# Kernel optimization log

Hardware: AMD Instinct MI355X
Metric: run time of the kernel (lower is better)

## Reference

```python
import jax, jax.numpy as jnp
import numpy as np

B, S, D, H = 2, 2048, 1024, 16
HD = D // H           # 64
AD = D // 8           # adapter dim 128


def setup_inputs() -> dict:
    key = jax.random.key(0)
    ks = jax.random.split(key, 16)
    s = 1.0 / np.sqrt(D)
    sa = 1.0 / np.sqrt(AD)
    return {
        "q": jax.random.normal(ks[0], (B, S, D), jnp.float32),
        "k": jax.random.normal(ks[1], (B, S, D), jnp.float32),
        "v": jax.random.normal(ks[2], (B, S, D), jnp.float32),
        "Wq": jax.random.normal(ks[3], (D, D), jnp.float32) * s,
        "bq": jnp.zeros((D,), jnp.float32),
        "Wk": jax.random.normal(ks[4], (D, D), jnp.float32) * s,
        "bk": jnp.zeros((D,), jnp.float32),
        "Wv": jax.random.normal(ks[5], (D, D), jnp.float32) * s,
        "bv": jnp.zeros((D,), jnp.float32),
        "Wo": jax.random.normal(ks[6], (D, D), jnp.float32) * s,
        "bo": jnp.zeros((D,), jnp.float32),
        "Wad": jax.random.normal(ks[7], (AD, D), jnp.float32) * s,
        "bad": jnp.zeros((AD,), jnp.float32),
        "Wau": jax.random.normal(ks[8], (D, AD), jnp.float32) * sa,
        "bau": jnp.zeros((D,), jnp.float32),
    }


def reference(q, k, v, Wq, bq, Wk, bk, Wv, bv, Wo, bo, Wad, bad, Wau, bau):
    # Linear projections (torch Linear: x @ W.T + b), split into heads
    def proj(x, W, b):
        y = jnp.einsum('bsd,ed->bse', x, W) + b
        return y.reshape(B, -1, H, HD).transpose(0, 2, 1, 3)  # [B,H,S,HD]

    qh, kh, vh = proj(q, Wq, bq), proj(k, Wk, bk), proj(v, Wv, bv)
    scores = jnp.einsum('bhqd,bhkd->bhqk', qh, kh) / np.sqrt(HD)  # [B,H,S,S]
    attn = jax.nn.softmax(scores, axis=-1)
    ctx = jnp.einsum('bhqk,bhkd->bhqd', attn, vh)
    ctx = ctx.transpose(0, 2, 1, 3).reshape(B, -1, D)  # [B,S,D]
    out = jnp.einsum('bsd,ed->bse', ctx, Wo) + bo
    # adapter: down -> GELU (exact erf) -> up, fused with residual
    a = jnp.einsum('bsd,ad->bsa', out, Wad) + bad
    a = jax.nn.gelu(a, approximate=False)
    a = jnp.einsum('bsa,da->bsd', a, Wau) + bau
    return out + a
```

## Files before the change

kernel.cpp:

```cpp
#include <hip/hip_runtime.h>
#include <hip/hip_bf16.h>
#include <math.h>

typedef __attribute__((ext_vector_type(8))) short short8;
typedef __attribute__((ext_vector_type(4))) float f32x4;

#define MFMA16(a,b,c) __builtin_amdgcn_mfma_f32_16x16x32_bf16((a),(b),(c),0,0,0)

__device__ __forceinline__ unsigned short f2bf(float f){
    union { __hip_bfloat16 b; unsigned short u; } cv;
    cv.b = __float2bfloat16(f);
    return cv.u;
}
__device__ __forceinline__ unsigned pk_bf16(float a, float b){
    unsigned r;
    asm("v_cvt_pk_bf16_f32 %0, %1, %2" : "=v"(r) : "v"(a), "v"(b));
    return r;
}
__device__ __forceinline__ float ex2(float x){
    return __builtin_amdgcn_exp2f(x);
}

#define GLD_LDS16(g, s) \
    __builtin_amdgcn_global_load_lds((const __attribute__((address_space(1))) void*)(g), \
                                     (__attribute__((address_space(3))) void*)(s), 16, 0, 0)

#define QSCALE 0.18033688011112042f
#define DEFER_THR 11.0f

struct CvtJobs {
    const float* src[6];
    unsigned short* dst[6];
    float scale[6];
    int n[6];
};

__global__ __launch_bounds__(256)
void convert_kernel(CvtJobs j, long long total4) {
    long long i4 = (long long)blockIdx.x * blockDim.x + threadIdx.x;
    if (i4 >= total4) return;
    long long rem = i4 * 4;
    int job = 0;
    while (job < 6 && rem >= j.n[job]) { rem -= j.n[job]; ++job; }
    if (job >= 6) return;
    const float sc = j.scale[job];
    const float4 v = *(const float4*)(j.src[job] + rem);
    ushort4 o;
    o.x = f2bf(v.x * sc); o.y = f2bf(v.y * sc);
    o.z = f2bf(v.z * sc); o.w = f2bf(v.w * sc);
    *(ushort4*)(j.dst[job] + rem) = o;
}

struct QKVArgs {
    const float* A[3];
    const unsigned short* W[3];
    const float* bias[3];
    float bscale[3];
    unsigned short* out[3];
};

__global__ __launch_bounds__(256)
void gemm_qkv(QKVArgs ar, int M, int N, int K)
{
    __shared__ float          Asf[2][128 * 32];
    __shared__ unsigned short Bs[2][128 * 32];

    const int z = blockIdx.z;
    const float* A = ar.A[z];
    const unsigned short* W = ar.W[z];
    const int tid = threadIdx.x;
    const int w = tid >> 6, l = tid & 63;
    const int lr = l & 15, lg = l >> 4;
    const int wr = w >> 1, wc = w & 1;
    const int m0 = blockIdx.x * 128, n0 = blockIdx.y * 128;
    const int ru = lg ^ ((lr >> 1) & 3);

    auto STAGE = [&](int bf, int k0) {
        #pragma unroll
        for (int c = 0; c < 4; ++c) {
            const int cid = c * 256 + tid;
            const int row = cid >> 3, u = cid & 7;
            const int su = u ^ (row & 7);
            GLD_LDS16((const char*)A + ((size_t)(m0 + row) * K + k0) * 4 + su * 16,
                      (char*)&Asf[bf][0] + (c * 256 + w * 64) * 16);
        }
        #pragma unroll
        for (int c = 0; c < 2; ++c) {
            const int cid = c * 256 + tid;
            const int row = cid >> 2, u = cid & 3;
            const int su = u ^ ((row >> 1) & 3);
            GLD_LDS16((const char*)W + ((size_t)(n0 + row) * K + k0) * 2 + su * 16,
                      (char*)&Bs[bf][0] + (c * 256 + w * 64) * 16);
        }
    };

    f32x4 acc[4][4] = {};
    STAGE(0, 0);
    __syncthreads();
    int cur = 0;

    for (int k0 = 0; k0 < K; k0 += 32) {
        if (k0 + 32 < K) STAGE(cur ^ 1, k0 + 32);

        short8 af[4], bfr[4];
        #pragma unroll
        for (int i = 0; i < 4; ++i) {
            const int row = wr * 64 + i * 16 + lr;
            const char* rb = (const char*)&Asf[cur][0] + row * 128;
            const float4 f0 = *(const float4*)(rb + (((lg * 2 + 0) ^ (row & 7)) * 16));
            const float4 f1 = *(const float4*)(rb + (((lg * 2 + 1) ^ (row & 7)) * 16));
            union { unsigned u[4]; short8 s; } cv;
            cv.u[0] = pk_bf16(f0.x, f0.y);
            cv.u[1] = pk_bf16(f0.z, f0.w);
            cv.u[2] = pk_bf16(f1.x, f1.y);
            cv.u[3] = pk_bf16(f1.z, f1.w);
            af[i] = cv.s;
        }
        #pragma unroll
        for (int jj = 0; jj < 4; ++jj)
            bfr[jj] = *(const short8*)((const char*)&Bs[cur][0] + (wc * 64 + jj * 16 + lr) * 64 + ru * 16);
        #pragma unroll
        for (int i = 0; i < 4; ++i)
            #pragma unroll
            for (int jj = 0; jj < 4; ++jj)
                acc[i][jj] = MFMA16(af[i], bfr[jj], acc[i][jj]);

        __syncthreads();
        cur ^= 1;
    }

    const float* bias = ar.bias[z];
    const float bsc = ar.bscale[z];
    unsigned short* out = ar.out[z];
    #pragma unroll
    for (int i = 0; i < 4; ++i)
        #pragma unroll
        for (int jj = 0; jj < 4; ++jj)
            #pragma unroll
            for (int r = 0; r < 4; ++r) {
                const int row = m0 + wr * 64 + i * 16 + lg * 4 + r;
                const int col = n0 + wc * 64 + jj * 16 + lr;
                const float c = acc[i][jj][r] + bias[col] * bsc;
                const int b = row >> 11, s = row & 2047, h = col >> 6, hd = col & 63;
                if (z < 2)
                    out[((((size_t)(b * 16 + h)) * 2048 + s) << 6) + hd] = f2bf(c);
                else
                    out[((((size_t)(b * 16 + h)) * 64 + hd) << 11) + s] = f2bf(c);
            }
}

template<int MODE>
__global__ __launch_bounds__(256)
void gemm_bf16(const unsigned short* __restrict__ A,
               const unsigned short* __restrict__ Wt,
               const float* __restrict__ bias,
               void* __restrict__ out0,
               void* __restrict__ out1,
               int M, int N, int K)
{
    __shared__ unsigned short As[2][128 * 32];
    __shared__ unsigned short Bs[2][128 * 32];

    const int tid = threadIdx.x;
    const int w = tid >> 6, l = tid & 63;
    const int lr = l & 15, lg = l >> 4;
    const int wr = w >> 1, wc = w & 1;
    const int m0 = blockIdx.x * 128, n0 = blockIdx.y * 128;
    const int ru = lg ^ ((lr >> 1) & 3);

    auto STAGE = [&](int bf, int k0) {
        #pragma unroll
        for (int c = 0; c < 2; ++c) {
            const int cid = c * 256 + tid;
            const int row = cid >> 2, u = cid & 3;
            const int su = u ^ ((row >> 1) & 3);
            GLD_LDS16((const char*)A  + ((size_t)(m0 + row) * K + k0) * 2 + su * 16,
                      (char*)&As[bf][0] + (c * 256 + w * 64) * 16);
            GLD_LDS16((const char*)Wt + ((size_t)(n0 + row) * K + k0) * 2 + su * 16,
                      (char*)&Bs[bf][0] + (c * 256 + w * 64) * 16);
        }
    };

    f32x4 acc[4][4] = {};
    STAGE(0, 0);
    __syncthreads();
    int cur = 0;

    for (int k0 = 0; k0 < K; k0 += 32) {
        if (k0 + 32 < K) STAGE(cur ^ 1, k0 + 32);

        short8 af[4], bfr[4];
        #pragma unroll
        for (int i = 0; i < 4; ++i)
            af[i] = *(const short8*)((const char*)&As[cur][0] + (wr * 64 + i * 16 + lr) * 64 + ru * 16);
        #pragma unroll
        for (int jj = 0; jj < 4; ++jj)
            bfr[jj] = *(const short8*)((const char*)&Bs[cur][0] + (wc * 64 + jj * 16 + lr) * 64 + ru * 16);
        #pragma unroll
        for (int i = 0; i < 4; ++i)
            #pragma unroll
            for (int jj = 0; jj < 4; ++jj)
                acc[i][jj] = MFMA16(af[i], bfr[jj], acc[i][jj]);

        __syncthreads();
        cur ^= 1;
    }

    #pragma unroll
    for (int i = 0; i < 4; ++i)
        #pragma unroll
        for (int jj = 0; jj < 4; ++jj)
            #pragma unroll
            for (int r = 0; r < 4; ++r) {
                const int row = m0 + wr * 64 + i * 16 + lg * 4 + r;
                const int col = n0 + wc * 64 + jj * 16 + lr;
                const float c = acc[i][jj][r] + bias[col];
                if (MODE == 2) {
                    ((float*)out0)[(size_t)row * N + col] = c;
                    ((unsigned short*)out1)[(size_t)row * N + col] = f2bf(c);
                } else {
                    ((float*)out0)[(size_t)row * N + col] =
                        c + ((const float*)out1)[(size_t)row * N + col];
                }
            }
}

__global__ __launch_bounds__(256)
void gemm64_gelu(const unsigned short* __restrict__ A,
                 const unsigned short* __restrict__ Wt,
                 const float* __restrict__ bias,
                 unsigned short* __restrict__ out,
                 int M, int N, int K)
{
    __shared__ unsigned short As[2][64 * 32];
    __shared__ unsigned short Bs[2][64 * 32];

    const int tid = threadIdx.x;
    const int w = tid >> 6, l = tid & 63;
    const int lr = l & 15, lg = l >> 4;
    const int wr = w >> 1, wc = w & 1;
    const int m0 = blockIdx.x * 64, n0 = blockIdx.y * 64;

    auto STAGE = [&](int bf, int k0) {
        const int row = tid >> 2, ch = tid & 3;
        GLD_LDS16(A  + (size_t)(m0 + row) * K + k0 + ch * 8, &As[bf][0] + (w * 64) * 8);
        GLD_LDS16(Wt + (size_t)(n0 + row) * K + k0 + ch * 8, &Bs[bf][0] + (w * 64) * 8);
    };

    f32x4 acc[2][2] = {};
    STAGE(0, 0);
    __syncthreads();
    int cur = 0;

    for (int k0 = 0; k0 < K; k0 += 32) {
        if (k0 + 32 < K) STAGE(cur ^ 1, k0 + 32);

        short8 af[2], bfr[2];
        #pragma unroll
        for (int i = 0; i < 2; ++i)
            af[i] = *(const short8*)(&As[cur][0] + ((wr * 32 + i * 16 + lr) * 32 + lg * 8));
        #pragma unroll
        for (int jj = 0; jj < 2; ++jj)
            bfr[jj] = *(const short8*)(&Bs[cur][0] + ((wc * 32 + jj * 16 + lr) * 32 + lg * 8));
        #pragma unroll
        for (int i = 0; i < 2; ++i)
            #pragma unroll
            for (int jj = 0; jj < 2; ++jj)
                acc[i][jj] = MFMA16(af[i], bfr[jj], acc[i][jj]);

        __syncthreads();
        cur ^= 1;
    }

    #pragma unroll
    for (int i = 0; i < 2; ++i)
        #pragma unroll
        for (int jj = 0; jj < 2; ++jj)
            #pragma unroll
            for (int r = 0; r < 4; ++r) {
                const int row = m0 + wr * 32 + i * 16 + lg * 4 + r;
                const int col = n0 + wc * 32 + jj * 16 + lr;
                const float c = acc[i][jj][r] + bias[col];
                const float g = 0.5f * c * (1.0f + erff(c * 0.70710678118654752f));
                out[(size_t)row * N + col] = f2bf(g);
            }
}

__global__ __launch_bounds__(512)
void attn_mfma(const unsigned short* __restrict__ Qh,
               const unsigned short* __restrict__ Kh,
               const unsigned short* __restrict__ Vt,
               unsigned short* __restrict__ ctx)
{
    __shared__ unsigned short Ks[2][64 * 64];
    __shared__ unsigned short Vs[2][64 * 64];
    __shared__ unsigned short Ps[8][16 * 64];

    const int tid = threadIdx.x;
    const int w = tid >> 6, l = tid & 63;
    const int lr = l & 15, lg = l >> 4;

    const int p = blockIdx.x + blockIdx.y * 16;
    const int id = (p & 7) * 64 + (p >> 3);
    const int q0 = (id & 15) << 7;
    const int bh = id >> 4;

    const unsigned short* Qb = Qh + (size_t)bh * 131072;
    const char* Kb = (const char*)(Kh + (size_t)bh * 131072);
    const char* Vb = (const char*)(Vt + (size_t)bh * 131072);

    short8 qf[2];
    #pragma unroll
    for (int c = 0; c < 2; ++c)
        qf[c] = *(const short8*)(Qb + (size_t)(q0 + w * 16 + lr) * 64 + c * 32 + lg * 8);

    float mrow = -1e30f;
    float lrow = 0.f;
    f32x4 accO[4] = {};

    auto STAGE = [&](int bf, int kt) {
        const int row = tid >> 3, u = tid & 7;
        const int su = u ^ (row & 7);
        GLD_LDS16(Kb + (size_t)(kt + row) * 128 + su * 16,
                  (char*)&Ks[bf][0] + (w * 64) * 16);
        GLD_LDS16(Vb + (size_t)row * 4096 + (size_t)kt * 2 + su * 16,
                  (char*)&Vs[bf][0] + (w * 64) * 16);
    };

    STAGE(0, 0);
    __syncthreads();

    int cur = 0;
    for (int t = 0; t < 32; ++t) {
        if (t < 31) STAGE(cur ^ 1, (t + 1) * 64);

        const char* Kbuf = (const char*)&Ks[cur][0];
        const char* Vbuf = (const char*)&Vs[cur][0];

        f32x4 sf[4] = {};
        __builtin_amdgcn_s_setprio(1);
        #pragma unroll
        for (int n = 0; n < 4; ++n) {
            const int krow = n * 16 + lr;
            const short8 kf0 = *(const short8*)(Kbuf + krow * 128 + ((0 * 4 + lg) ^ (lr & 7)) * 16);
            const short8 kf1 = *(const short8*)(Kbuf + krow * 128 + ((1 * 4 + lg) ^ (lr & 7)) * 16);
            sf[n] = MFMA16(kf0, qf[0], sf[n]);
            sf[n] = MFMA16(kf1, qf[1], sf[n]);
        }
        __builtin_amdgcn_s_setprio(0);

        short8 vf[4][2];
        #pragma unroll
        for (int n = 0; n < 4; ++n) {
            const int drow = n * 16 + lr;
            vf[n][0] = *(const short8*)(Vbuf + drow * 128 + ((0 * 4 + lg) ^ (lr & 7)) * 16);
            vf[n][1] = *(const short8*)(Vbuf + drow * 128 + ((1 * 4 + lg) ^ (lr & 7)) * 16);
        }

        float a = fmaxf(fmaxf(fmaxf(sf[0][0], sf[0][1]), fmaxf(sf[0][2], sf[0][3])),
                        fmaxf(fmaxf(sf[1][0], sf[1][1]), fmaxf(sf[1][2], sf[1][3])));
        float b2 = fmaxf(fmaxf(fmaxf(sf[2][0], sf[2][1]), fmaxf(sf[2][2], sf[2][3])),
                         fmaxf(fmaxf(sf[3][0], sf[3][1]), fmaxf(sf[3][2], sf[3][3])));
        float r2 = fmaxf(a, b2);
        r2 = fmaxf(r2, __shfl_xor(r2, 16));
        r2 = fmaxf(r2, __shfl_xor(r2, 32));
        const bool need = (r2 > mrow + DEFER_THR);
        if (__any(need)) {
            const float mnew = fmaxf(mrow, r2);
            const float rsc = ex2(mrow - mnew);
            lrow *= rsc;
            mrow = mnew;
            #pragma unroll
            for (int r = 0; r < 4; ++r) {
                const float rr = __shfl(rsc, (l & 48) | (lg * 4 + r));
                #pragma unroll
                for (int n = 0; n < 4; ++n) accO[n][r] *= rr;
            }
        }
        {
            const float m = mrow;
            float ls = lrow;
            char* pbase = (char*)&Ps[w][0] + lr * 128;
            #pragma unroll
            for (int n = 0; n < 4; ++n) {
                const float p0 = ex2(sf[n][0] - m);
                const float p1 = ex2(sf[n][1] - m);
                const float p2 = ex2(sf[n][2] - m);
                const float p3 = ex2(sf[n][3] - m);
                ls += (p0 + p1) + (p2 + p3);
                uint2 pk;
                pk.x = pk_bf16(p0, p1);
                pk.y = pk_bf16(p2, p3);
                *(uint2*)(pbase + (((n * 2 + (lg >> 1)) ^ (lr & 7)) * 16) + (lg & 1) * 8) = pk;
            }
            lrow = ls;
        }

        asm volatile("" ::: "memory");

        short8 pf[2];
        {
            const char* pb = (const char*)&Ps[w][0] + lr * 128;
            #pragma unroll
            for (int c = 0; c < 2; ++c) {
                union { uint2 q2[2]; short8 s8; } cvt;
                const char* base = pb + (((c * 4 + lg) ^ (lr & 7)) * 16);
                cvt.q2[0] = *(const uint2*)(base);
                cvt.q2[1] = *(const uint2*)(base + 8);
                pf[c] = cvt.s8;
            }
        }

        __builtin_amdgcn_s_setprio(1);
        #pragma unroll
        for (int n = 0; n < 4; ++n) {
            accO[n] = MFMA16(pf[0], vf[n][0], accO[n]);
            accO[n] = MFMA16(pf[1], vf[n][1], accO[n]);
        }
        __builtin_amdgcn_s_setprio(0);

        __syncthreads();
        cur ^= 1;
    }

    const int b = bh >> 4, h = bh & 15;
    {
        float ls = lrow;
        ls += __shfl_xor(ls, 16);
        ls += __shfl_xor(ls, 32);
        const float inv = 1.0f / ls;
        #pragma unroll
        for (int r = 0; r < 4; ++r) {
            const float vr = __shfl(inv, (l & 48) | (lg * 4 + r));
            const int srow = q0 + w * 16 + lg * 4 + r;
            const size_t base = ((size_t)b * 2048 + srow) * 1024 + h * 64;
            #pragma unroll
            for (int n = 0; n < 4; ++n)
                ctx[base + n * 16 + lr] = f2bf(accO[n][r] * vr);
        }
    }
}

extern "C" void kernel_launch(void* const* d_in, const int* in_sizes, int n_in,
                              void* d_out, int out_size, void* d_ws, size_t ws_size,
                              hipStream_t stream) {
    const float* q   = (const float*)d_in[0];
    const float* k   = (const float*)d_in[1];
    const float* v   = (const float*)d_in[2];
    const float* Wq  = (const float*)d_in[3];
    const float* bq  = (const float*)d_in[4];
    const float* Wk  = (const float*)d_in[5];
    const float* bk  = (const float*)d_in[6];
    const float* Wv  = (const float*)d_in[7];
    const float* bv  = (const float*)d_in[8];
    const float* Wo  = (const float*)d_in[9];
    const float* bo  = (const float*)d_in[10];
    const float* Wad = (const float*)d_in[11];
    const float* bad = (const float*)d_in[12];
    const float* Wau = (const float*)d_in[13];
    const float* bau = (const float*)d_in[14];

    const int M = 4096, D = 1024, AD = 128;
    const size_t SZ = (size_t)M * D;

    char* p = (char*)d_ws;
    size_t off = 0;
    auto alloc = [&](size_t bytes) { void* r = p + off; off = (off + bytes + 255) & ~(size_t)255; return r; };
    unsigned short* Wqb  = (unsigned short*)alloc((size_t)D * D * 2);
    unsigned short* Wkb  = (unsigned short*)alloc((size_t)D * D * 2);
    unsigned short* Wvb  = (unsigned short*)alloc((size_t)D * D * 2);
    unsigned short* Wob  = (unsigned short*)alloc((size_t)D * D * 2);
    unsigned short* Wadb = (unsigned short*)alloc((size_t)AD * D * 2);
    unsigned short* Waub = (unsigned short*)alloc((size_t)D * AD * 2);
    unsigned short* Qh   = (unsigned short*)alloc(SZ * 2);
    unsigned short* Kh   = (unsigned short*)alloc(SZ * 2);
    unsigned short* Vt   = (unsigned short*)alloc(SZ * 2);
    unsigned short* ctx  = (unsigned short*)alloc(SZ * 2);
    float*          outp = (float*)alloc(SZ * 4);
    unsigned short* outb = (unsigned short*)alloc(SZ * 2);
    unsigned short* a1   = (unsigned short*)alloc((size_t)M * AD * 2);

    CvtJobs j;
    j.src[0] = Wq;  j.dst[0] = Wqb;  j.n[0] = D * D;   j.scale[0] = QSCALE;
    j.src[1] = Wk;  j.dst[1] = Wkb;  j.n[1] = D * D;   j.scale[1] = 1.f;
    j.src[2] = Wv;  j.dst[2] = Wvb;  j.n[2] = D * D;   j.scale[2] = 1.f;
    j.src[3] = Wo;  j.dst[3] = Wob;  j.n[3] = D * D;   j.scale[3] = 1.f;
    j.src[4] = Wad; j.dst[4] = Wadb; j.n[4] = AD * D;  j.scale[4] = 1.f;
    j.src[5] = Wau; j.dst[5] = Waub; j.n[5] = D * AD;  j.scale[5] = 1.f;
    long long total = 4LL * D * D + 2LL * AD * D;
    long long total4 = total / 4;
    convert_kernel<<<dim3((unsigned)((total4 + 255) / 256)), dim3(256), 0, stream>>>(j, total4);

    const dim3 blk(256);

    QKVArgs qa;
    qa.A[0] = q;   qa.A[1] = k;   qa.A[2] = v;
    qa.W[0] = Wqb; qa.W[1] = Wkb; qa.W[2] = Wvb;
    qa.bias[0] = bq; qa.bias[1] = bk; qa.bias[2] = bv;
    qa.bscale[0] = QSCALE; qa.bscale[1] = 1.f; qa.bscale[2] = 1.f;
    qa.out[0] = Qh; qa.out[1] = Kh; qa.out[2] = Vt;
    gemm_qkv<<<dim3(M / 128, D / 128, 3), blk, 0, stream>>>(qa, M, D, D);

    attn_mfma<<<dim3(16, 32), dim3(512), 0, stream>>>(Qh, Kh, Vt, ctx);

    gemm_bf16<2><<<dim3(M / 128, D / 128), blk, 0, stream>>>(ctx, Wob, bo, outp, outb, M, D, D);
    gemm64_gelu<<<dim3(M / 64, AD / 64), blk, 0, stream>>>(outb, Wadb, bad, a1, M, AD, D);
    gemm_bf16<4><<<dim3(M / 128, D / 128), blk, 0, stream>>>(a1, Waub, bau, d_out, outp, M, D, AD);
}
```

Before: 153.4 us.

## Load QKV GEMM operands directly from global memory, dropping LDS staging

```diff
diff --git a/kernel.cpp b/kernel.cpp
--- a/kernel.cpp
+++ b/kernel.cpp
@@ -62,9 +62,6 @@
 __global__ __launch_bounds__(256)
 void gemm_qkv(QKVArgs ar, int M, int N, int K)
 {
-    __shared__ float          Asf[2][128 * 32];
-    __shared__ unsigned short Bs[2][128 * 32];
-
     const int z = blockIdx.z;
     const float* A = ar.A[z];
     const unsigned short* W = ar.W[z];
@@ -73,42 +70,24 @@
     const int lr = l & 15, lg = l >> 4;
     const int wr = w >> 1, wc = w & 1;
     const int m0 = blockIdx.x * 128, n0 = blockIdx.y * 128;
-    const int ru = lg ^ ((lr >> 1) & 3);
-
-    auto STAGE = [&](int bf, int k0) {
-        #pragma unroll
-        for (int c = 0; c < 4; ++c) {
-            const int cid = c * 256 + tid;
-            const int row = cid >> 3, u = cid & 7;
-            const int su = u ^ (row & 7);
-            GLD_LDS16((const char*)A + ((size_t)(m0 + row) * K + k0) * 4 + su * 16,
-                      (char*)&Asf[bf][0] + (c * 256 + w * 64) * 16);
-        }
-        #pragma unroll
-        for (int c = 0; c < 2; ++c) {
-            const int cid = c * 256 + tid;
-            const int row = cid >> 2, u = cid & 3;
-            const int su = u ^ ((row >> 1) & 3);
-            GLD_LDS16((const char*)W + ((size_t)(n0 + row) * K + k0) * 2 + su * 16,
-                      (char*)&Bs[bf][0] + (c * 256 + w * 64) * 16);
-        }
-    };
+
+    const float* Ab[4];
+    const unsigned short* Wb[4];
+    #pragma unroll
+    for (int i = 0; i < 4; ++i) {
+        Ab[i] = A + (size_t)(m0 + wr * 64 + i * 16 + lr) * K + lg * 8;
+        Wb[i] = W + (size_t)(n0 + wc * 64 + i * 16 + lr) * K + lg * 8;
+    }
 
     f32x4 acc[4][4] = {};
-    STAGE(0, 0);
-    __syncthreads();
-    int cur = 0;
 
     for (int k0 = 0; k0 < K; k0 += 32) {
-        if (k0 + 32 < K) STAGE(cur ^ 1, k0 + 32);
-
         short8 af[4], bfr[4];
         #pragma unroll
         for (int i = 0; i < 4; ++i) {
-            const int row = wr * 64 + i * 16 + lr;
-            const char* rb = (const char*)&Asf[cur][0] + row * 128;
-            const float4 f0 = *(const float4*)(rb + (((lg * 2 + 0) ^ (row & 7)) * 16));
-            const float4 f1 = *(const float4*)(rb + (((lg * 2 + 1) ^ (row & 7)) * 16));
+            const float4 f0 = *(const float4*)(Ab[i] + k0);
+            const float4 f1 = *(const float4*)(Ab[i] + k0 + 4);
+            bfr[i] = *(const short8*)(Wb[i] + k0);
             union { unsigned u[4]; short8 s; } cv;
             cv.u[0] = pk_bf16(f0.x, f0.y);
             cv.u[1] = pk_bf16(f0.z, f0.w);
@@ -117,16 +96,10 @@
             af[i] = cv.s;
         }
         #pragma unroll
-        for (int jj = 0; jj < 4; ++jj)
-            bfr[jj] = *(const short8*)((const char*)&Bs[cur][0] + (wc * 64 + jj * 16 + lr) * 64 + ru * 16);
-        #pragma unroll
         for (int i = 0; i < 4; ++i)
             #pragma unroll
             for (int jj = 0; jj < 4; ++jj)
                 acc[i][jj] = MFMA16(af[i], bfr[jj], acc[i][jj]);
-
-        __syncthreads();
-        cur ^= 1;
     }
 
     const float* bias = ar.bias[z];
```

Result: slower. 245.1 us (+59.8%).
